# Kernel tuning notes

Hardware: AMD Instinct MI355X
Metric: run time of the kernel (lower is better)

The kernel has to match this reference:

```python
import jax, jax.numpy as jnp
import numpy as np

EMBED = 1024
HEADS = 16
HEAD_DIM = EMBED // HEADS


def setup_inputs() -> dict:
    key = jax.random.key(0)
    ks = jax.random.split(key, 7)
    B, S = 2, 2048
    return {
        "key": jax.random.normal(ks[0], (B, S, EMBED), dtype=jnp.float32),
        "query": jax.random.normal(ks[1], (B, S, EMBED), dtype=jnp.float32),
        "value": jax.random.normal(ks[2], (B, S, EMBED), dtype=jnp.float32),
        "Wk": jax.random.normal(ks[3], (EMBED, EMBED), dtype=jnp.float32) * (EMBED ** -0.5),
        "Wq": jax.random.normal(ks[4], (EMBED, EMBED), dtype=jnp.float32) * (EMBED ** -0.5),
        "Wv": jax.random.normal(ks[5], (EMBED, EMBED), dtype=jnp.float32) * (EMBED ** -0.5),
        "Wo": jax.random.normal(ks[6], (EMBED, EMBED), dtype=jnp.float32) * (EMBED ** -0.5),
        "mask": 1,
    }


def _split_heads(x):
    B, S, _ = x.shape
    return x.reshape(B, S, HEADS, HEAD_DIM).transpose(0, 2, 1, 3)  # (B,H,S,D)


def reference(key, query, value, Wk, Wq, Wv, Wo, mask):
    # torch Linear (no bias): y = x @ W.T
    k = _split_heads(key @ Wk.T)
    q = _split_heads(query @ Wq.T)
    v = _split_heads(value @ Wv.T)
    # NOTE: module scales by sqrt(embed_dims), not sqrt(head_dims)
    scale = 1.0 / jnp.sqrt(jnp.float32(EMBED))
    scores = jnp.einsum('bhqd,bhkd->bhqk', q, k) * scale  # (B,H,S,S)
    S = scores.shape[-1]
    if mask:
        # triu(full(-100000), diagonal=1).type(int) -> exactly -100000 above diag
        causal = jnp.triu(jnp.full((S, S), -100000.0, dtype=jnp.float32), k=1)
        scores = scores + causal
    attn = jax.nn.softmax(scores, axis=-1)
    out = jnp.einsum('bhqk,bhkd->bhqd', attn, v)  # (B,H,S,D)
    B = out.shape[0]
    out = out.transpose(0, 2, 1, 3).reshape(B, S, EMBED)
    return out @ Wo.T
```

## Files before the change

### kernel.cpp

```cpp
#include <hip/hip_runtime.h>
#include <hip/hip_bf16.h>

typedef unsigned short u16;
typedef __attribute__((ext_vector_type(8))) short bf16x8;
typedef __attribute__((ext_vector_type(4))) float f32x4;

#define GLDS16(g, l)                                                        \
  __builtin_amdgcn_global_load_lds(                                         \
      (const __attribute__((address_space(1))) void*)(g),                   \
      (__attribute__((address_space(3))) void*)(l), 16, 0, 0)

__device__ __forceinline__ u16 f2bf(float f) {
  union { float f; unsigned u; } v; v.f = f;
  unsigned r = v.u + 0x7FFFu + ((v.u >> 16) & 1u);
  return (u16)(r >> 16);
}

__global__ __launch_bounds__(256) void cvt_all(
    const float4* __restrict__ a0, const float4* __restrict__ a1,
    const float4* __restrict__ a2, const float4* __restrict__ a3,
    const float4* __restrict__ a4, const float4* __restrict__ a5,
    const float4* __restrict__ a6, ushort4* __restrict__ b0,
    ushort4* __restrict__ b1, ushort4* __restrict__ b2,
    ushort4* __restrict__ b3, ushort4* __restrict__ b4,
    ushort4* __restrict__ b5, ushort4* __restrict__ b6) {
  int bid = blockIdx.x;
  const float4* s; ushort4* d; int off;
  if (bid < 4096)       { s = a0; d = b0; off = bid; }
  else if (bid < 8192)  { s = a1; d = b1; off = bid - 4096; }
  else if (bid < 12288) { s = a2; d = b2; off = bid - 8192; }
  else if (bid < 13312) { s = a3; d = b3; off = bid - 12288; }
  else if (bid < 14336) { s = a4; d = b4; off = bid - 13312; }
  else if (bid < 15360) { s = a5; d = b5; off = bid - 14336; }
  else                  { s = a6; d = b6; off = bid - 15360; }
  int i = off * 256 + threadIdx.x;
  float4 v = s[i];
  ushort4 o;
  o.x = f2bf(v.x); o.y = f2bf(v.y); o.z = f2bf(v.z); o.w = f2bf(v.w);
  d[i] = o;
}

template <int MODE>
__device__ __forceinline__ void gemm_core(const u16* __restrict__ A,
                                          const u16* __restrict__ W,
                                          void* __restrict__ C) {
  const int K = 1024;
  __shared__ u16 lds_a[4096];
  __shared__ u16 lds_b[4096];
  const int bn = blockIdx.x, bm = blockIdx.y;
  const int tid = threadIdx.x, l = tid & 63, wid = tid >> 6;
  const int wr = wid >> 1, wc = wid & 1;
  const int l4 = l >> 4, l15 = l & 15;

  f32x4 zero4 = {0.f, 0.f, 0.f, 0.f};
  f32x4 acc[4][4];
  for (int i = 0; i < 4; ++i)
    for (int j = 0; j < 4; ++j) acc[i][j] = zero4;

  const int srow = tid >> 2, scol = (tid & 3) * 8;
  const u16* Ag = A + (bm * 128 + srow) * K + scol;
  const u16* Wg = W + (bn * 128 + srow) * K + scol;
  char* la = (char*)lds_a + wid * 1024;
  char* lb = (char*)lds_b + wid * 1024;

  for (int kt = 0; kt < K; kt += 32) {
    GLDS16(Ag + kt, la);
    GLDS16(Ag + 64 * K + kt, la + 4096);
    GLDS16(Wg + kt, lb);
    GLDS16(Wg + 64 * K + kt, lb + 4096);
    __syncthreads();
    bf16x8 af[4], bf[4];
    for (int i = 0; i < 4; ++i)
      af[i] = *(const bf16x8*)((const char*)lds_a +
                               (wr * 64 + i * 16 + l15) * 64 + l4 * 16);
    for (int j = 0; j < 4; ++j)
      bf[j] = *(const bf16x8*)((const char*)lds_b +
                               (wc * 64 + j * 16 + l15) * 64 + l4 * 16);
    for (int i = 0; i < 4; ++i)
      for (int j = 0; j < 4; ++j)
        acc[i][j] = __builtin_amdgcn_mfma_f32_16x16x32_bf16(af[i], bf[j],
                                                            acc[i][j], 0, 0, 0);
    __syncthreads();
  }

  for (int i = 0; i < 4; ++i)
    for (int j = 0; j < 4; ++j) {
      f32x4 a = acc[i][j];
      for (int r = 0; r < 4; ++r) {
        int m = bm * 128 + wr * 64 + i * 16 + l4 * 4 + r;
        int n = bn * 128 + wc * 64 + j * 16 + l15;
        if (MODE == 0) {
          int bb = m >> 11, srw = m & 2047, h = n >> 6, d = n & 63;
          ((u16*)C)[((bb * 16 + h) * 2048 + srw) * 64 + d] = f2bf(a[r]);
        } else {
          ((float*)C)[m * 1024 + n] = a[r];
        }
      }
    }
}

__global__ __launch_bounds__(256) void gemm_proj(
    const u16* __restrict__ X0, const u16* __restrict__ X1,
    const u16* __restrict__ X2, const u16* __restrict__ W0,
    const u16* __restrict__ W1, const u16* __restrict__ W2,
    u16* __restrict__ O0, u16* __restrict__ O1, u16* __restrict__ O2) {
  int z = blockIdx.z;
  const u16* A = (z == 0) ? X0 : (z == 1) ? X1 : X2;
  const u16* W = (z == 0) ? W0 : (z == 1) ? W1 : W2;
  u16* O = (z == 0) ? O0 : (z == 1) ? O1 : O2;
  gemm_core<0>(A, W, (void*)O);
}

__global__ __launch_bounds__(256) void gemm_out(const u16* __restrict__ A,
                                                const u16* __restrict__ W,
                                                float* __restrict__ C) {
  gemm_core<1>(A, W, (void*)C);
}

__global__ __launch_bounds__(256) void transpose_v(const u16* __restrict__ Vp,
                                                   u16* __restrict__ Vt) {
  const int st = blockIdx.x, bh = blockIdx.y;
  const int d = threadIdx.x & 63, sg = threadIdx.x >> 6;
  const u16* src = Vp + bh * 131072;
  u16* dst = Vt + bh * 131072;
  const int s0 = st * 64 + sg * 16;
  u16 tmp[16];
  for (int i = 0; i < 16; ++i) tmp[i] = src[(s0 + i) * 64 + d];
  ushort4* o = (ushort4*)(dst + d * 2048 + s0);
  for (int k = 0; k < 4; ++k) {
    ushort4 t4;
    t4.x = tmp[4 * k]; t4.y = tmp[4 * k + 1];
    t4.z = tmp[4 * k + 2]; t4.w = tmp[4 * k + 3];
    o[k] = t4;
  }
}

__global__ __launch_bounds__(256, 2) void attn_kernel(
    const u16* __restrict__ Qp, const u16* __restrict__ Kp,
    const u16* __restrict__ Vt, u16* __restrict__ ctx) {
  const int bid = blockIdx.x;
  const int logical = ((bid & 7) << 6) | (bid >> 3);
  const int x = logical & 15, bh = logical >> 4;
  const int tid = threadIdx.x, w = tid >> 6, l = tid & 63;
  const int l4 = l >> 4, l15 = l & 15;
  __shared__ u16 lds_p[4][1024];
  char* pw = (char*)lds_p[w];

  const u16* Qbh = Qp + bh * 131072;
  const u16* Kbh = Kp + bh * 131072;
  const u16* Vbh = Vt + bh * 131072;
  const int b = bh >> 4, h = bh & 15;
  u16* ctxb = ctx + (size_t)b * 2048 * 1024 + h * 64;

  const float SCALE2 = 0.03125f * 1.44269504f;
  const float PEN2 = 144269.5f;
  const int swz = (l15 & 7) << 4;

  auto LOADK = [&](bf16x8* kf, int t) {
    const u16* kb = Kbh + (t * 64 + l15) * 64 + l4 * 8;
    for (int g = 0; g < 4; ++g) {
      kf[g] = *(const bf16x8*)(kb + g * 1024);
      kf[g + 4] = *(const bf16x8*)(kb + g * 1024 + 32);
    }
  };
  auto LOADV = [&](bf16x8* vf, int t) {
    const u16* vb = Vbh + l15 * 2048 + t * 64 + l4 * 8;
    for (int g = 0; g < 4; ++g) {
      vf[g] = *(const bf16x8*)(vb + g * 16 * 2048);
      vf[g + 4] = *(const bf16x8*)(vb + g * 16 * 2048 + 32);
    }
  };

  for (int half = 0; half < 2; ++half) {
    const int qt = half ? (31 - x) : x;
    const int q0 = qt * 64 + w * 16;

    const u16* qb = Qbh + (q0 + l15) * 64 + l4 * 8;
    const bf16x8 bq0 = *(const bf16x8*)(qb);
    const bf16x8 bq1 = *(const bf16x8*)(qb + 32);

    f32x4 zero4 = {0.f, 0.f, 0.f, 0.f};
    f32x4 accO[4];
    for (int g = 0; g < 4; ++g) accO[g] = zero4;
    float m2 = -1.0e30f, lsum = 0.f;

    auto BODY = [&](const bf16x8* kf, const bf16x8* vf, int t2) {
      const int kv0 = t2 * 64;
      f32x4 s[4];
      for (int g = 0; g < 4; ++g)
        s[g] = __builtin_amdgcn_mfma_f32_16x16x32_bf16(kf[g], bq0, zero4,
                                                       0, 0, 0);
      for (int g = 0; g < 4; ++g)
        s[g] = __builtin_amdgcn_mfma_f32_16x16x32_bf16(kf[g + 4], bq1, s[g],
                                                       0, 0, 0);
      float sv[4][4];
      if (t2 == qt) {
        const int q = q0 + l15;
        for (int g = 0; g < 4; ++g)
          for (int r = 0; r < 4; ++r) {
            int kv = kv0 + g * 16 + l4 * 4 + r;
            sv[g][r] = s[g][r] * SCALE2 - (kv > q ? PEN2 : 0.f);
          }
      } else {
        for (int g = 0; g < 4; ++g)
          for (int r = 0; r < 4; ++r) sv[g][r] = s[g][r] * SCALE2;
      }
      float mx = sv[0][0];
      for (int g = 0; g < 4; ++g)
        for (int r = 0; r < 4; ++r) mx = fmaxf(mx, sv[g][r]);
      mx = fmaxf(mx, __shfl_xor(mx, 16));
      mx = fmaxf(mx, __shfl_xor(mx, 32));
      const float mnew = fmaxf(m2, mx);
      const float alpha = __builtin_exp2f(m2 - mnew);
      m2 = mnew;
      float p[4][4], rs = 0.f;
      for (int g = 0; g < 4; ++g)
        for (int r = 0; r < 4; ++r) {
          float e = __builtin_exp2f(sv[g][r] - mnew);
          p[g][r] = e;
          rs += e;
        }
      rs += __shfl_xor(rs, 16);
      rs += __shfl_xor(rs, 32);
      lsum = lsum * alpha + rs;
      float aR[4];
      for (int r = 0; r < 4; ++r) aR[r] = __shfl(alpha, l4 * 4 + r);
      for (int g = 0; g < 4; ++g) {
        f32x4 t = accO[g];
        t[0] *= aR[0]; t[1] *= aR[1]; t[2] *= aR[2]; t[3] *= aR[3];
        accO[g] = t;
      }
      for (int g = 0; g < 4; ++g) {
        ushort4 q4;
        q4.x = f2bf(p[g][0]); q4.y = f2bf(p[g][1]);
        q4.z = f2bf(p[g][2]); q4.w = f2bf(p[g][3]);
        int byte = (l15 * 128 + g * 32 + l4 * 8) ^ swz;
        *(ushort4*)(pw + byte) = q4;
      }
      bf16x8 pa0 = *(const bf16x8*)(pw + ((l15 * 128 + l4 * 16) ^ swz));
      bf16x8 pa1 = *(const bf16x8*)(pw + ((l15 * 128 + 64 + l4 * 16) ^ swz));
      for (int g = 0; g < 4; ++g)
        accO[g] = __builtin_amdgcn_mfma_f32_16x16x32_bf16(pa0, vf[g],
                                                          accO[g], 0, 0, 0);
      for (int g = 0; g < 4; ++g)
        accO[g] = __builtin_amdgcn_mfma_f32_16x16x32_bf16(pa1, vf[g + 4],
                                                          accO[g], 0, 0, 0);
    };

    bf16x8 k0[8], v0[8], k1[8], v1[8];
    LOADK(k0, 0); LOADV(v0, 0);
    int t2 = 0;
    while (true) {
      if (t2 < qt) { LOADK(k1, t2 + 1); LOADV(v1, t2 + 1); }
      BODY(k0, v0, t2);
      if (++t2 > qt) break;
      if (t2 < qt) { LOADK(k0, t2 + 1); LOADV(v0, t2 + 1); }
      BODY(k1, v1, t2);
      if (++t2 > qt) break;
    }

    float inv[4];
    for (int r = 0; r < 4; ++r) inv[r] = 1.f / __shfl(lsum, l4 * 4 + r);
    for (int r = 0; r < 4; ++r) {
      u16* orow = ctxb + (size_t)(q0 + l4 * 4 + r) * 1024;
      for (int g = 0; g < 4; ++g)
        orow[g * 16 + l15] = f2bf(accO[g][r] * inv[r]);
    }
  }
}

extern "C" void kernel_launch(void* const* d_in, const int* in_sizes, int n_in,
                              void* d_out, int out_size, void* d_ws,
                              size_t ws_size, hipStream_t stream) {
  (void)in_sizes; (void)n_in; (void)out_size; (void)ws_size;
  const float* key = (const float*)d_in[0];
  const float* query = (const float*)d_in[1];
  const float* value = (const float*)d_in[2];
  const float* Wk = (const float*)d_in[3];
  const float* Wq = (const float*)d_in[4];
  const float* Wv = (const float*)d_in[5];
  const float* Wo = (const float*)d_in[6];

  char* ws = (char*)d_ws;
  u16* keyb = (u16*)(ws + 0);
  u16* qryb = (u16*)(ws + 8388608);
  u16* valb = (u16*)(ws + 16777216);
  u16* Wkb  = (u16*)(ws + 25165824);
  u16* Wqb  = (u16*)(ws + 27262976);
  u16* Wvb  = (u16*)(ws + 29360128);
  u16* Wob  = (u16*)(ws + 31457280);
  u16* Kp   = (u16*)(ws + 33554432);
  u16* Qp   = (u16*)(ws + 41943040);
  u16* Vp   = (u16*)(ws + 50331648);
  u16* Vt   = (u16*)(ws + 58720256);
  u16* ctx  = (u16*)(ws + 67108864);

  cvt_all<<<16384, 256, 0, stream>>>(
      (const float4*)key, (const float4*)query, (const float4*)value,
      (const float4*)Wk, (const float4*)Wq, (const float4*)Wv,
      (const float4*)Wo, (ushort4*)keyb, (ushort4*)qryb, (ushort4*)valb,
      (ushort4*)Wkb, (ushort4*)Wqb, (ushort4*)Wvb, (ushort4*)Wob);

  gemm_proj<<<dim3(8, 32, 3), 256, 0, stream>>>(keyb, qryb, valb, Wkb, Wqb,
                                                Wvb, Kp, Qp, Vp);
  transpose_v<<<dim3(32, 32), 256, 0, stream>>>(Vp, Vt);
  attn_kernel<<<512, 256, 0, stream>>>(Qp, Kp, Vt, ctx);
  gemm_out<<<dim3(8, 32), 256, 0, stream>>>(ctx, Wob, (float*)d_out);
}
```

Before: 314.4 us.

## Split attention KV loop across two waves with LDS merge of partial softmax

Restructures the attention kernel so each 128-thread block handles one 16-row query strip for two paired q-tiles. The two waves split the KV tiles even/odd and merge their partial max, sum and output through shared memory at the end. This gives 2048 smaller blocks for better load balance and more parallelism, and it interleaves two independent softmax chains per wave. Cross-lane reductions now use permlane swap intrinsics where they are available. The explicit register double-buffering of K/V is dropped, and the causal mask is applied on every tile, which adds ALU work and the cost of the merge step.

```diff
diff --git a/kernel.cpp b/kernel.cpp
--- a/kernel.cpp
+++ b/kernel.cpp
@@ -14,6 +14,52 @@
   union { float f; unsigned u; } v; v.f = f;
   unsigned r = v.u + 0x7FFFu + ((v.u >> 16) & 1u);
   return (u16)(r >> 16);
+}
+
+__device__ __forceinline__ float rowquad_max(float v) {
+#if __has_builtin(__builtin_amdgcn_permlane16_swap) && \
+    __has_builtin(__builtin_amdgcn_permlane32_swap)
+  unsigned u = __builtin_bit_cast(unsigned, v);
+  {
+    auto r = __builtin_amdgcn_permlane16_swap(u, u, false, false);
+    v = fmaxf(__builtin_bit_cast(float, (unsigned)r[0]),
+              __builtin_bit_cast(float, (unsigned)r[1]));
+  }
+  u = __builtin_bit_cast(unsigned, v);
+  {
+    auto r = __builtin_amdgcn_permlane32_swap(u, u, false, false);
+    v = fmaxf(__builtin_bit_cast(float, (unsigned)r[0]),
+              __builtin_bit_cast(float, (unsigned)r[1]));
+  }
+  return v;
+#else
+  v = fmaxf(v, __shfl_xor(v, 16));
+  v = fmaxf(v, __shfl_xor(v, 32));
+  return v;
+#endif
+}
+
+__device__ __forceinline__ float rowquad_sum(float v) {
+#if __has_builtin(__builtin_amdgcn_permlane16_swap) && \
+    __has_builtin(__builtin_amdgcn_permlane32_swap)
+  unsigned u = __builtin_bit_cast(unsigned, v);
+  {
+    auto r = __builtin_amdgcn_permlane16_swap(u, u, false, false);
+    v = __builtin_bit_cast(float, (unsigned)r[0]) +
+        __builtin_bit_cast(float, (unsigned)r[1]);
+  }
+  u = __builtin_bit_cast(unsigned, v);
+  {
+    auto r = __builtin_amdgcn_permlane32_swap(u, u, false, false);
+    v = __builtin_bit_cast(float, (unsigned)r[0]) +
+        __builtin_bit_cast(float, (unsigned)r[1]);
+  }
+  return v;
+#else
+  v += __shfl_xor(v, 16);
+  v += __shfl_xor(v, 32);
+  return v;
+#endif
 }
 
 __global__ __launch_bounds__(256) void cvt_all(
@@ -135,16 +181,20 @@
   }
 }
 
-__global__ __launch_bounds__(256, 2) void attn_kernel(
+__global__ __launch_bounds__(128, 4) void attn_kernel(
     const u16* __restrict__ Qp, const u16* __restrict__ Kp,
     const u16* __restrict__ Vt, u16* __restrict__ ctx) {
   const int bid = blockIdx.x;
-  const int logical = ((bid & 7) << 6) | (bid >> 3);
-  const int x = logical & 15, bh = logical >> 4;
-  const int tid = threadIdx.x, w = tid >> 6, l = tid & 63;
+  const int logical = ((bid & 7) << 8) | (bid >> 3);
+  const int bh = logical >> 6;
+  const int rem = logical & 63;
+  const int s = rem >> 4, x = rem & 15;
+  const int tid = threadIdx.x, w01 = tid >> 6, l = tid & 63;
   const int l4 = l >> 4, l15 = l & 15;
-  __shared__ u16 lds_p[4][1024];
-  char* pw = (char*)lds_p[w];
+
+  __shared__ u16 psl[2][2][1024];
+  __shared__ float OxA[16][64], OxB[16][64];
+  __shared__ f32x4 mlA[2][2][4], mlB[2][2][4];
 
   const u16* Qbh = Qp + bh * 131072;
   const u16* Kbh = Kp + bh * 131072;
@@ -155,118 +205,167 @@
   const float SCALE2 = 0.03125f * 1.44269504f;
   const float PEN2 = 144269.5f;
   const int swz = (l15 & 7) << 4;
-
-  auto LOADK = [&](bf16x8* kf, int t) {
-    const u16* kb = Kbh + (t * 64 + l15) * 64 + l4 * 8;
+  const f32x4 zero4 = {0.f, 0.f, 0.f, 0.f};
+
+  const int pA = w01, pB = 1 - w01;
+  const int qtA = x, qtB = 31 - x;
+  const int q0A = qtA * 64 + s * 16, q0B = qtB * 64 + s * 16;
+
+  const u16* qbA = Qbh + (q0A + l15) * 64 + l4 * 8;
+  const bf16x8 bqA0 = *(const bf16x8*)(qbA);
+  const bf16x8 bqA1 = *(const bf16x8*)(qbA + 32);
+  const u16* qbB = Qbh + (q0B + l15) * 64 + l4 * 8;
+  const bf16x8 bqB0 = *(const bf16x8*)(qbB);
+  const bf16x8 bqB1 = *(const bf16x8*)(qbB + 32);
+
+  f32x4 accA[4], accB[4];
+  for (int g = 0; g < 4; ++g) { accA[g] = zero4; accB[g] = zero4; }
+  float mA = -1.0e30f, lA = 0.f, mB = -1.0e30f, lB = 0.f;
+
+  auto BODY = [&](f32x4 (&acc)[4], float& m2, float& lsum, const bf16x8 bq0,
+                  const bf16x8 bq1, const int q0, const int t, u16* slab) {
+    const int kv0 = t * 64;
+    char* pw = (char*)slab;
+    const u16* kb = Kbh + (kv0 + l15) * 64 + l4 * 8;
+    bf16x8 kf[8];
+#pragma unroll
     for (int g = 0; g < 4; ++g) {
       kf[g] = *(const bf16x8*)(kb + g * 1024);
       kf[g + 4] = *(const bf16x8*)(kb + g * 1024 + 32);
     }
-  };
-  auto LOADV = [&](bf16x8* vf, int t) {
-    const u16* vb = Vbh + l15 * 2048 + t * 64 + l4 * 8;
+    const u16* vb = Vbh + l15 * 2048 + kv0 + l4 * 8;
+    bf16x8 vf[8];
+#pragma unroll
     for (int g = 0; g < 4; ++g) {
       vf[g] = *(const bf16x8*)(vb + g * 16 * 2048);
       vf[g + 4] = *(const bf16x8*)(vb + g * 16 * 2048 + 32);
     }
+    f32x4 sacc[4];
+#pragma unroll
+    for (int g = 0; g < 4; ++g)
+      sacc[g] = __builtin_amdgcn_mfma_f32_16x16x32_bf16(kf[g], bq0, zero4,
+                                                        0, 0, 0);
+#pragma unroll
+    for (int g = 0; g < 4; ++g)
+      sacc[g] = __builtin_amdgcn_mfma_f32_16x16x32_bf16(kf[g + 4], bq1,
+                                                        sacc[g], 0, 0, 0);
+    const int qk = q0 + l15 - kv0;
+    float sv[4][4];
+#pragma unroll
+    for (int g = 0; g < 4; ++g)
+#pragma unroll
+      for (int r = 0; r < 4; ++r) {
+        int kvl = g * 16 + l4 * 4 + r;
+        sv[g][r] = sacc[g][r] * SCALE2 - (kvl > qk ? PEN2 : 0.f);
+      }
+    float mx = sv[0][0];
+#pragma unroll
+    for (int g = 0; g < 4; ++g)
+#pragma unroll
+      for (int r = 0; r < 4; ++r) mx = fmaxf(mx, sv[g][r]);
+    mx = rowquad_max(mx);
+    const float mnew = fmaxf(m2, mx);
+    const float alpha = __builtin_exp2f(m2 - mnew);
+    m2 = mnew;
+    float aR[4];
+#pragma unroll
+    for (int r = 0; r < 4; ++r) aR[r] = __shfl(alpha, l4 * 4 + r);
+    float p[4][4], rs = 0.f;
+#pragma unroll
+    for (int g = 0; g < 4; ++g)
+#pragma unroll
+      for (int r = 0; r < 4; ++r) {
+        float e = __builtin_exp2f(sv[g][r] - mnew);
+        p[g][r] = e;
+        rs += e;
+      }
+    rs = rowquad_sum(rs);
+    lsum = lsum * alpha + rs;
+#pragma unroll
+    for (int g = 0; g < 4; ++g) {
+      f32x4 t4 = acc[g];
+      t4[0] *= aR[0]; t4[1] *= aR[1]; t4[2] *= aR[2]; t4[3] *= aR[3];
+      acc[g] = t4;
+    }
+#pragma unroll
+    for (int g = 0; g < 4; ++g) {
+      ushort4 q4;
+      q4.x = f2bf(p[g][0]); q4.y = f2bf(p[g][1]);
+      q4.z = f2bf(p[g][2]); q4.w = f2bf(p[g][3]);
+      int byte = (l15 * 128 + g * 32 + l4 * 8) ^ swz;
+      *(ushort4*)(pw + byte) = q4;
+    }
+    bf16x8 pa0 = *(const bf16x8*)(pw + ((l15 * 128 + l4 * 16) ^ swz));
+    bf16x8 pa1 = *(const bf16x8*)(pw + ((l15 * 128 + 64 + l4 * 16) ^ swz));
+#pragma unroll
+    for (int g = 0; g < 4; ++g)
+      acc[g] = __builtin_amdgcn_mfma_f32_16x16x32_bf16(pa0, vf[g], acc[g],
+                                                       0, 0, 0);
+#pragma unroll
+    for (int g = 0; g < 4; ++g)
+      acc[g] = __builtin_amdgcn_mfma_f32_16x16x32_bf16(pa1, vf[g + 4], acc[g],
+                                                       0, 0, 0);
   };
 
-  for (int half = 0; half < 2; ++half) {
-    const int qt = half ? (31 - x) : x;
-    const int q0 = qt * 64 + w * 16;
-
-    const u16* qb = Qbh + (q0 + l15) * 64 + l4 * 8;
-    const bf16x8 bq0 = *(const bf16x8*)(qb);
-    const bf16x8 bq1 = *(const bf16x8*)(qb + 32);
-
-    f32x4 zero4 = {0.f, 0.f, 0.f, 0.f};
-    f32x4 accO[4];
-    for (int g = 0; g < 4; ++g) accO[g] = zero4;
-    float m2 = -1.0e30f, lsum = 0.f;
-
-    auto BODY = [&](const bf16x8* kf, const bf16x8* vf, int t2) {
-      const int kv0 = t2 * 64;
-      f32x4 s[4];
-      for (int g = 0; g < 4; ++g)
-        s[g] = __builtin_amdgcn_mfma_f32_16x16x32_bf16(kf[g], bq0, zero4,
-                                                       0, 0, 0);
-      for (int g = 0; g < 4; ++g)
-        s[g] = __builtin_amdgcn_mfma_f32_16x16x32_bf16(kf[g + 4], bq1, s[g],
-                                                       0, 0, 0);
-      float sv[4][4];
-      if (t2 == qt) {
-        const int q = q0 + l15;
-        for (int g = 0; g < 4; ++g)
-          for (int r = 0; r < 4; ++r) {
-            int kv = kv0 + g * 16 + l4 * 4 + r;
-            sv[g][r] = s[g][r] * SCALE2 - (kv > q ? PEN2 : 0.f);
-          }
-      } else {
-        for (int g = 0; g < 4; ++g)
-          for (int r = 0; r < 4; ++r) sv[g][r] = s[g][r] * SCALE2;
+  const int rAmax = (x - pA) >> 1;
+  const int rmax = (31 - x - pB) >> 1;
+  int r = 0;
+  for (; r <= rAmax; ++r) {
+    BODY(accA, mA, lA, bqA0, bqA1, q0A, 2 * r + pA, &psl[w01][0][0]);
+    BODY(accB, mB, lB, bqB0, bqB1, q0B, 2 * r + pB, &psl[w01][1][0]);
+  }
+  for (; r <= rmax; ++r)
+    BODY(accB, mB, lB, bqB0, bqB1, q0B, 2 * r + pB, &psl[w01][1][0]);
+
+  if (l < 16) {
+    ((float*)&mlA[w01][0][0])[l] = mA;
+    ((float*)&mlA[w01][1][0])[l] = lA;
+    ((float*)&mlB[w01][0][0])[l] = mB;
+    ((float*)&mlB[w01][1][0])[l] = lB;
+  }
+  if (w01 == 1) {
+#pragma unroll
+    for (int g = 0; g < 4; ++g)
+#pragma unroll
+      for (int rr = 0; rr < 4; ++rr) OxA[g * 4 + rr][l] = accA[g][rr];
+  } else {
+#pragma unroll
+    for (int g = 0; g < 4; ++g)
+#pragma unroll
+      for (int rr = 0; rr < 4; ++rr) OxB[g * 4 + rr][l] = accB[g][rr];
+  }
+  __syncthreads();
+
+  auto MERGE = [&](const f32x4 (&acc)[4], const f32x4 (&ml)[2][2][4],
+                   const float* Ox, const int q0) {
+    const f32x4 mO = ml[w01][0][l4];
+    const f32x4 lO = ml[w01][1][l4];
+    const f32x4 mP = ml[w01 ^ 1][0][l4];
+    const f32x4 lP = ml[w01 ^ 1][1][l4];
+    float wO[4], wP[4], inv[4];
+#pragma unroll
+    for (int rr = 0; rr < 4; ++rr) {
+      float mN = fmaxf(mO[rr], mP[rr]);
+      wO[rr] = __builtin_exp2f(mO[rr] - mN);
+      wP[rr] = __builtin_exp2f(mP[rr] - mN);
+      float ln = lO[rr] * wO[rr] + lP[rr] * wP[rr];
+      inv[rr] = 1.f / ln;
+    }
+#pragma unroll
+    for (int rr = 0; rr < 4; ++rr) {
+      u16* orow = ctxb + (size_t)(q0 + l4 * 4 + rr) * 1024;
+#pragma unroll
+      for (int g = 0; g < 4; ++g) {
+        float po = Ox[(g * 4 + rr) * 64 + l];
+        float val = (acc[g][rr] * wO[rr] + po * wP[rr]) * inv[rr];
+        orow[g * 16 + l15] = f2bf(val);
       }
-      float mx = sv[0][0];
-      for (int g = 0; g < 4; ++g)
-        for (int r = 0; r < 4; ++r) mx = fmaxf(mx, sv[g][r]);
-      mx = fmaxf(mx, __shfl_xor(mx, 16));
-      mx = fmaxf(mx, __shfl_xor(mx, 32));
-      const float mnew = fmaxf(m2, mx);
-      const float alpha = __builtin_exp2f(m2 - mnew);
-      m2 = mnew;
-      float p[4][4], rs = 0.f;
-      for (int g = 0; g < 4; ++g)
-        for (int r = 0; r < 4; ++r) {
-          float e = __builtin_exp2f(sv[g][r] - mnew);
-          p[g][r] = e;
-          rs += e;
-        }
-      rs += __shfl_xor(rs, 16);
-      rs += __shfl_xor(rs, 32);
-      lsum = lsum * alpha + rs;
-      float aR[4];
-      for (int r = 0; r < 4; ++r) aR[r] = __shfl(alpha, l4 * 4 + r);
-      for (int g = 0; g < 4; ++g) {
-        f32x4 t = accO[g];
-        t[0] *= aR[0]; t[1] *= aR[1]; t[2] *= aR[2]; t[3] *= aR[3];
-        accO[g] = t;
-      }
-      for (int g = 0; g < 4; ++g) {
-        ushort4 q4;
-        q4.x = f2bf(p[g][0]); q4.y = f2bf(p[g][1]);
-        q4.z = f2bf(p[g][2]); q4.w = f2bf(p[g][3]);
-        int byte = (l15 * 128 + g * 32 + l4 * 8) ^ swz;
-        *(ushort4*)(pw + byte) = q4;
-      }
-      bf16x8 pa0 = *(const bf16x8*)(pw + ((l15 * 128 + l4 * 16) ^ swz));
-      bf16x8 pa1 = *(const bf16x8*)(pw + ((l15 * 128 + 64 + l4 * 16) ^ swz));
-      for (int g = 0; g < 4; ++g)
-        accO[g] = __builtin_amdgcn_mfma_f32_16x16x32_bf16(pa0, vf[g],
-                                                          accO[g], 0, 0, 0);
-      for (int g = 0; g < 4; ++g)
-        accO[g] = __builtin_amdgcn_mfma_f32_16x16x32_bf16(pa1, vf[g + 4],
-                                                          accO[g], 0, 0, 0);
-    };
-
-    bf16x8 k0[8], v0[8], k1[8], v1[8];
-    LOADK(k0, 0); LOADV(v0, 0);
-    int t2 = 0;
-    while (true) {
-      if (t2 < qt) { LOADK(k1, t2 + 1); LOADV(v1, t2 + 1); }
-      BODY(k0, v0, t2);
-      if (++t2 > qt) break;
-      if (t2 < qt) { LOADK(k0, t2 + 1); LOADV(v0, t2 + 1); }
-      BODY(k1, v1, t2);
-      if (++t2 > qt) break;
-    }
-
-    float inv[4];
-    for (int r = 0; r < 4; ++r) inv[r] = 1.f / __shfl(lsum, l4 * 4 + r);
-    for (int r = 0; r < 4; ++r) {
-      u16* orow = ctxb + (size_t)(q0 + l4 * 4 + r) * 1024;
-      for (int g = 0; g < 4; ++g)
-        orow[g * 16 + l15] = f2bf(accO[g][r] * inv[r]);
-    }
-  }
+    }
+  };
+  if (w01 == 0)
+    MERGE(accA, mlA, &OxA[0][0], q0A);
+  else
+    MERGE(accB, mlB, &OxB[0][0], q0B);
 }
 
 extern "C" void kernel_launch(void* const* d_in, const int* in_sizes, int n_in,
@@ -304,6 +403,6 @@
   gemm_proj<<<dim3(8, 32, 3), 256, 0, stream>>>(keyb, qryb, valb, Wkb, Wqb,
                                                 Wvb, Kp, Qp, Vp);
   transpose_v<<<dim3(32, 32), 256, 0, stream>>>(Vp, Vt);
-  attn_kernel<<<512, 256, 0, stream>>>(Qp, Kp, Vt, ctx);
+  attn_kernel<<<2048, 128, 0, stream>>>(Qp, Kp, Vt, ctx);
   gemm_out<<<dim3(8, 32), 256, 0, stream>>>(ctx, Wob, (float*)d_out);
 }
```

After: 319.8 us. About the same (+1.7%).
